# Performance work log

Hardware: AMD Instinct MI355X
Metric: run time of the kernel (lower is better)

## Reference

```python
import jax, jax.numpy as jnp
import numpy as np

N_REACH = 4096
N_T = 730
DT = 3600.0
VEL_LB = 0.3
VEL_UB = 15.0
Q_LB = 1e-4
SLOPE_LB = 1e-4


def _make_adjacency(n):
    # River-network DAG in topological order: each reach j (except outlet)
    # drains to exactly one downstream reach i > j  =>  strictly lower-triangular.
    rng = np.random.default_rng(0)
    j = np.arange(n - 1)
    ds = j + 1 + (rng.random(n - 1) * (n - 1 - j)).astype(np.int64)
    adj = np.zeros((n, n), dtype=np.float32)
    adj[ds, j] = 1.0
    return jnp.asarray(adj)


def setup_inputs() -> dict:
    key = jax.random.key(0)
    ks = jax.random.split(key, 8)
    u = lambda k, s: jax.random.uniform(k, s, dtype=jnp.float32)
    q_prime = u(ks[0], (N_T, N_REACH)) * 10.0            # lateral inflow m^3/s
    n = 0.01 + 0.09 * u(ks[1], (N_REACH,))               # Manning's n
    q_spatial = 1.5 + u(ks[2], (N_REACH,))               # log base > 1
    p_spatial = 1.0 + 3.0 * u(ks[3], (N_REACH,))         # width scale
    length = 1000.0 + 5000.0 * u(ks[4], (N_REACH,))      # reach length [m]
    slope = 1e-3 + 0.05 * u(ks[5], (N_REACH,))           # channel slope
    width = 5.0 + 100.0 * u(ks[6], (N_REACH,))           # width > p_spatial
    x_storage = 0.1 + 0.3 * u(ks[7], (N_REACH,))         # Muskingum x
    adj = _make_adjacency(N_REACH)
    return {"q_prime": q_prime, "n": n, "q_spatial": q_spatial,
            "p_spatial": p_spatial, "length": length, "slope": slope,
            "width": width, "x_storage": x_storage, "adj": adj}


def reference(q_prime, n, q_spatial, p_spatial, length, slope, width, x_storage, adj):
    slope = jnp.clip(slope, SLOPE_LB)
    # Manning's equation -> celerity (note: independent of discharge, as in source)
    depth = jnp.log(width / p_spatial) / jnp.log(q_spatial)
    v = (1.0 / n) * depth ** (2.0 / 3.0) * jnp.sqrt(slope)
    c = jnp.clip(v, VEL_LB, VEL_UB) * (5.0 / 3.0)
    k = length / c
    denom = 2.0 * k * (1.0 - x_storage) + DT
    c1 = (DT - 2.0 * k * x_storage) / denom
    c2 = (DT + 2.0 * k * x_storage) / denom
    c3 = (2.0 * k * (1.0 - x_storage) - DT) / denom
    c4 = 2.0 * DT / denom

    # Lower-triangular routing system: A = I - diag(c1) @ adjacency (constant)
    N = q_prime.shape[1]
    A = jnp.eye(N, dtype=q_prime.dtype) - c1[:, None] * adj

    q0 = q_prime[0]
    out0 = jnp.clip(q0[-1], Q_LB)  # single gage at index -1

    def step(q_t, qp_row):
        q_l = jnp.clip(qp_row, Q_LB)
        i_t = adj @ q_t                        # upstream inflow
        b = c2 * i_t + c3 * q_t + c4 * q_l
        x = jax.scipy.linalg.solve_triangular(A, b[:, None], lower=True)[:, 0]
        q_t1 = jnp.clip(x, Q_LB)
        return q_t1, q_t1[-1]

    _, outs = jax.lax.scan(step, q0, q_prime[:-1])  # timesteps 1..T-1 use q_prime[t-1]
    runoff = jnp.concatenate([out0[None], outs])[None, :]  # [1, T]
    return runoff
```

## Files before the change

### kernel.cpp

```cpp
#include <hip/hip_runtime.h>

#define N 4096
#define NT 730
#define NTH 512
#define PER_T 8
#define QLB 1e-4f
#define DT_S 3600.0f

#define WS_DS     0
#define WS_SZ     4096
#define WS_CCNT   8192
#define WS_COFF   12288
#define WS_CUR    16388
#define WS_HI     20484
#define WS_FLAG   24580
#define WS_C1     28676
#define WS_C2     32772
#define WS_C3     36868
#define WS_C4     40964
#define WS_CLIST  45060
#define WS_GP     49156
#define WS_LOP    53252
#define WS_C3P    57348
#define WS_C4P    61444
#define WS_CCNTP  65540
#define WS_COFF2  69636
#define WS_CUR2   73736
#define WS_EQ     77832
#define WS_EW     81928
#define WS_SP     86024
#define WS_ISP    94216
#define WS_QPP    102408
#define WS_END    (WS_QPP + NT * N)

__device__ __forceinline__ int qidx(int p) { return ((p & 7) << 9) | (p >> 3); }

template <int CTRL, int RMASK>
__device__ __forceinline__ double dpp_stage(double v) {
    union U { double d; unsigned int u[2]; };
    U s, t;
    s.d = v;
    t.u[0] = (unsigned)__builtin_amdgcn_update_dpp(0, (int)s.u[0], CTRL, RMASK, 0xf, false);
    t.u[1] = (unsigned)__builtin_amdgcn_update_dpp(0, (int)s.u[1], CTRL, RMASK, 0xf, false);
    return v + t.d;
}
__device__ __forceinline__ double wave_incl_scan(double v) {
    v = dpp_stage<0x111, 0xf>(v);
    v = dpp_stage<0x112, 0xf>(v);
    v = dpp_stage<0x114, 0xf>(v);
    v = dpp_stage<0x118, 0xf>(v);
    v = dpp_stage<0x142, 0xa>(v);
    v = dpp_stage<0x143, 0xc>(v);
    return v;
}

__global__ void k_init(int* ds, int* sz, int* ccnt, int* hi, int* flag) {
    int j = blockIdx.x * 256 + threadIdx.x;
    if (j < N) { ds[j] = N - 1; sz[j] = 1; ccnt[j] = 0; hi[j] = -1; flag[j] = 0; }
}

__global__ void k_extract(const float4* __restrict__ adj4, int* __restrict__ ds) {
    long idx = (long)blockIdx.x * 256 + threadIdx.x;
    if (idx >= (long)N * N / 4) return;
    float4 w = adj4[idx];
    long base = idx * 4;
    int row = (int)(base >> 12);
    int col = (int)(base & 4095);
    if (w.x != 0.0f) ds[col + 0] = row;
    if (w.y != 0.0f) ds[col + 1] = row;
    if (w.z != 0.0f) ds[col + 2] = row;
    if (w.w != 0.0f) ds[col + 3] = row;
}

__global__ void k_coeffs(const float* n, const float* qs, const float* ps,
                         const float* len, const float* slope, const float* width,
                         const float* xs, float* __restrict__ c1, float* __restrict__ c2,
                         float* __restrict__ c3, float* __restrict__ c4) {
    int i = blockIdx.x * 256 + threadIdx.x;
    if (i >= N) return;
    float s  = fmaxf(slope[i], 1e-4f);
    float dp = logf(width[i] / ps[i]) / logf(qs[i]);
    float v  = (1.0f / n[i]) * powf(dp, 2.0f / 3.0f) * sqrtf(s);
    float c  = fminf(fmaxf(v, 0.3f), 15.0f) * (5.0f / 3.0f);
    float k  = len[i] / c;
    float x  = xs[i];
    float denom = 2.0f * k * (1.0f - x) + DT_S;
    c1[i] = (DT_S - 2.0f * k * x) / denom;
    c2[i] = (DT_S + 2.0f * k * x) / denom;
    c3[i] = (2.0f * k * (1.0f - x) - DT_S) / denom;
    c4[i] = 2.0f * DT_S / denom;
}

__global__ void k_count(const int* __restrict__ ds, int* __restrict__ ccnt,
                        int* __restrict__ sz) {
    int u = blockIdx.x * 256 + threadIdx.x;
    if (u >= N || u == N - 1) return;
    atomicAdd(&ccnt[ds[u]], 1);
    int a = ds[u];
    while (true) {
        atomicAdd(&sz[a], 1);
        if (a == N - 1) break;
        a = ds[a];
    }
}

__global__ __launch_bounds__(1024) void k_scan(const int* __restrict__ src,
                                               int* __restrict__ off,
                                               int* __restrict__ cur) {
    __shared__ int buf[1024];
    int tid = threadIdx.x;
    int a0 = src[tid * 4 + 0], a1 = src[tid * 4 + 1];
    int a2 = src[tid * 4 + 2], a3 = src[tid * 4 + 3];
    int s1 = a0, s2 = a0 + a1, s3 = a0 + a1 + a2, tot = s3 + a3;
    buf[tid] = tot;
    __syncthreads();
    for (int o = 1; o < 1024; o <<= 1) {
        int add = (tid >= o) ? buf[tid - o] : 0;
        __syncthreads();
        buf[tid] += add;
        __syncthreads();
    }
    int base = buf[tid] - tot;
    off[tid * 4 + 0] = base;      cur[tid * 4 + 0] = base;
    off[tid * 4 + 1] = base + s1; cur[tid * 4 + 1] = base + s1;
    off[tid * 4 + 2] = base + s2; cur[tid * 4 + 2] = base + s2;
    off[tid * 4 + 3] = base + s3; cur[tid * 4 + 3] = base + s3;
    if (tid == 1023) off[N] = buf[1023];
}

__global__ void k_fill(const int* __restrict__ ds, int* __restrict__ cur,
                       int* __restrict__ clist) {
    int u = blockIdx.x * 256 + threadIdx.x;
    if (u >= N || u == N - 1) return;
    int cp = atomicAdd(&cur[ds[u]], 1);
    clist[cp] = u;
}

__global__ __launch_bounds__(1024) void k_post(const int* __restrict__ ds,
                                               const int* __restrict__ sz,
                                               const int* __restrict__ coff,
                                               const int* __restrict__ ccnt,
                                               const int* __restrict__ clist,
                                               int* __restrict__ hi,
                                               int* __restrict__ flag) {
    int tid = threadIdx.x;
    if (tid == 0) hi[N - 1] = N - 1;
    __syncthreads();
    for (int it = 0; it < 96; ++it) {
        for (int v = tid; v < N; v += 1024) {
            if (hi[v] >= 0 && flag[v] == 0) {
                int cum = hi[v] - sz[v] + 1;
                int b0 = coff[v], e0 = b0 + ccnt[v];
                for (int k = b0; k < e0; ++k) {
                    int c = clist[k];
                    hi[c] = cum + sz[c] - 1;
                    cum += sz[c];
                }
                flag[v] = 1;
            }
        }
        __syncthreads();
    }
}

__global__ void k_prep(const int* __restrict__ ds, const int* __restrict__ sz,
                       const int* __restrict__ ccnt, const int* __restrict__ hi,
                       const float* __restrict__ c1, const float* __restrict__ c3,
                       const float* __restrict__ c4,
                       int* __restrict__ gP, int* __restrict__ loP,
                       float* __restrict__ c3P, float* __restrict__ c4P,
                       int* __restrict__ ccntP,
                       double* __restrict__ SP, double* __restrict__ ISP) {
    int u = blockIdx.x * 256 + threadIdx.x;
    if (u >= N) return;
    int p = hi[u];
    double s = 1.0;
    if (u != N - 1) {
        int a = ds[u];
        while (true) {
            s *= (double)c1[a];
            if (a == N - 1) break;
            a = ds[a];
        }
    }
    SP[p] = s; ISP[p] = 1.0 / s;
    gP[p] = u;
    loP[p] = p - sz[u] + 1;
    c3P[p] = c3[u]; c4P[p] = c4[u];
    ccntP[p] = ccnt[u];
}

__global__ void k_fill2(const int* __restrict__ ds, const int* __restrict__ hi,
                        const float* __restrict__ c2, int* __restrict__ cur2,
                        unsigned int* __restrict__ EQ, float* __restrict__ EW) {
    int u = blockIdx.x * 256 + threadIdx.x;
    if (u >= N) return;
    if (u == N - 1) {
        unsigned rq = (unsigned)qidx(N - 1);
        EQ[N - 1] = (rq << 12) | rq;
        EW[N - 1] = 0.0f;
        return;
    }
    int d = ds[u];
    int slot = atomicAdd(&cur2[hi[d]], 1);
    EQ[slot] = ((unsigned)qidx(hi[u]) << 12) | (unsigned)qidx(hi[d]);
    EW[slot] = c2[d];
}

__global__ void k_permute(const float* __restrict__ qp, const int* __restrict__ gP,
                          float* __restrict__ qpp) {
    long e = (long)blockIdx.x * 256 + threadIdx.x;
    if (e >= (long)NT * N) return;
    int tr = (int)(e >> 12);
    int v  = (int)(e & 4095);
    qpp[e] = qp[(size_t)tr * N + gP[v]];
}

__global__ __launch_bounds__(NTH) void k_route(
    const float* __restrict__ qp, const float* __restrict__ qpp,
    const float* __restrict__ c3g, const float* __restrict__ c4g,
    const int* __restrict__ gPg, const int* __restrict__ loPg,
    const double* __restrict__ SPg, const double* __restrict__ ISPg,
    const unsigned int* __restrict__ EQg, const float* __restrict__ EWg,
    int use_perm, float* __restrict__ out) {
    __shared__ float qL[N];
    __shared__ float CS[N];
    __shared__ double TL[N];
    __shared__ __align__(16) double wpart[8];
    int tid = threadIdx.x;
    int lane = tid & 63, wid = tid >> 6;

    unsigned int eq[PER_T];
    float ew[PER_T];
    int lo[PER_T], g[PER_T];
    float c3r[PER_T], c4r[PER_T], qreg[PER_T], qn[PER_T];
    double Sr[PER_T], iSr[PER_T];
#pragma unroll
    for (int r = 0; r < PER_T; ++r) {
        int p = tid * PER_T + r;
        eq[r] = EQg[p]; ew[r] = EWg[p];
        lo[r] = loPg[p]; g[r] = gPg[p];
        c3r[r] = c3g[p]; c4r[r] = c4g[p];
        Sr[r] = SPg[p]; iSr[r] = ISPg[p];
        float q0 = use_perm ? qpp[p] : qp[g[r]];
        qreg[r] = q0;
        qL[(r << 9) | tid] = q0;
        CS[(r << 9) | tid] = c3r[r] * q0 + c4r[r] * fmaxf(q0, QLB);
    }
    if (tid == NTH - 1) out[0] = fmaxf(qreg[PER_T - 1], QLB);
    __syncthreads();

    for (int t = 1; t < NT; ++t) {
#pragma unroll
        for (int e = 0; e < PER_T; ++e) {
            float qv = qL[eq[e] >> 12];
            atomicAdd(&CS[eq[e] & 4095u], ew[e] * qv);
        }
        __syncthreads();
        float bb[PER_T];
        double yv[PER_T], Tloc[PER_T];
        double tl = 0.0;
#pragma unroll
        for (int r = 0; r < PER_T; ++r) {
            float b = CS[(r << 9) | tid];
            bb[r] = b;
            double y = Sr[r] * (double)b;
            yv[r] = y;
            tl += y;
            Tloc[r] = tl;
        }
        double incl = wave_incl_scan(tl);
        if (lane == 63) wpart[wid] = incl;
        __syncthreads();
        double2 w0 = *(const double2*)&wpart[0];
        double2 w1 = *(const double2*)&wpart[2];
        double2 w2 = *(const double2*)&wpart[4];
        double2 w3 = *(const double2*)&wpart[6];
        double woff = 0.0;
        if (wid > 0) woff += w0.x;
        if (wid > 1) woff += w0.y;
        if (wid > 2) woff += w1.x;
        if (wid > 3) woff += w1.y;
        if (wid > 4) woff += w2.x;
        if (wid > 5) woff += w2.y;
        if (wid > 6) woff += w3.x;
        double texcl = woff + incl - tl;
#pragma unroll
        for (int r = 0; r < PER_T; ++r)
            TL[(r << 9) | tid] = texcl + Tloc[r];
        __syncthreads();
        if (t < NT - 1) {
            if (use_perm) {
                const float4* row4 = (const float4*)(qpp + (size_t)t * N);
                float4 a = row4[tid * 2], b = row4[tid * 2 + 1];
                qn[0] = a.x; qn[1] = a.y; qn[2] = a.z; qn[3] = a.w;
                qn[4] = b.x; qn[5] = b.y; qn[6] = b.z; qn[7] = b.w;
            } else {
                const float* row = qp + (size_t)t * N;
#pragma unroll
                for (int r = 0; r < PER_T; ++r) qn[r] = row[g[r]];
            }
        }
#pragma unroll
        for (int r = 0; r < PER_T; ++r) {
            int l = lo[r];
            double Tg = (l > 0) ? TL[qidx(l - 1)] : 0.0;
            double Tself = texcl + Tloc[r] - yv[r];
            double x = (double)bb[r] + (Tself - Tg) * iSr[r];
            qreg[r] = fmaxf((float)x, QLB);
        }
        if (tid == NTH - 1) out[t] = qreg[PER_T - 1];
#pragma unroll
        for (int r = 0; r < PER_T; ++r) {
            qL[(r << 9) | tid] = qreg[r];
            CS[(r << 9) | tid] = c3r[r] * qreg[r] + c4r[r] * fmaxf(qn[r], QLB);
        }
        __syncthreads();
    }
}

extern "C" void kernel_launch(void* const* d_in, const int* in_sizes, int n_in,
                              void* d_out, int out_size, void* d_ws, size_t ws_size,
                              hipStream_t stream) {
    const float* qp    = (const float*)d_in[0];
    const float* n     = (const float*)d_in[1];
    const float* qs    = (const float*)d_in[2];
    const float* ps    = (const float*)d_in[3];
    const float* len   = (const float*)d_in[4];
    const float* slope = (const float*)d_in[5];
    const float* width = (const float*)d_in[6];
    const float* xs    = (const float*)d_in[7];
    const float* adj   = (const float*)d_in[8];
    float* out = (float*)d_out;

    int*          W     = (int*)d_ws;
    int*          ds    = W + WS_DS;
    int*          sz    = W + WS_SZ;
    int*          ccnt  = W + WS_CCNT;
    int*          coff  = W + WS_COFF;
    int*          cur   = W + WS_CUR;
    int*          hi    = W + WS_HI;
    int*          flag  = W + WS_FLAG;
    float*        c1    = (float*)(W + WS_C1);
    float*        c2    = (float*)(W + WS_C2);
    float*        c3    = (float*)(W + WS_C3);
    float*        c4    = (float*)(W + WS_C4);
    int*          clist = W + WS_CLIST;
    int*          gP    = W + WS_GP;
    int*          loP   = W + WS_LOP;
    float*        c3P   = (float*)(W + WS_C3P);
    float*        c4P   = (float*)(W + WS_C4P);
    int*          ccntP = W + WS_CCNTP;
    int*          coff2 = W + WS_COFF2;
    int*          cur2  = W + WS_CUR2;
    unsigned int* EQ    = (unsigned int*)(W + WS_EQ);
    float*        EW    = (float*)(W + WS_EW);
    double*       SP    = (double*)(W + WS_SP);
    double*       ISP   = (double*)(W + WS_ISP);
    float*        QPP   = (float*)(W + WS_QPP);

    int use_perm = (ws_size >= (size_t)WS_END * 4) ? 1 : 0;

    k_init<<<(N + 255) / 256, 256, 0, stream>>>(ds, sz, ccnt, hi, flag);
    k_extract<<<(N * N / 4 + 255) / 256, 256, 0, stream>>>((const float4*)adj, ds);
    k_coeffs<<<(N + 255) / 256, 256, 0, stream>>>(n, qs, ps, len, slope, width, xs,
                                                  c1, c2, c3, c4);
    k_count<<<(N + 255) / 256, 256, 0, stream>>>(ds, ccnt, sz);
    k_scan<<<1, 1024, 0, stream>>>(ccnt, coff, cur);
    k_fill<<<(N + 255) / 256, 256, 0, stream>>>(ds, cur, clist);
    k_post<<<1, 1024, 0, stream>>>(ds, sz, coff, ccnt, clist, hi, flag);
    k_prep<<<(N + 255) / 256, 256, 0, stream>>>(ds, sz, ccnt, hi, c1, c3, c4,
                                                gP, loP, c3P, c4P, ccntP, SP, ISP);
    k_scan<<<1, 1024, 0, stream>>>(ccntP, coff2, cur2);
    k_fill2<<<(N + 255) / 256, 256, 0, stream>>>(ds, hi, c2, cur2, EQ, EW);
    if (use_perm)
        k_permute<<<(int)(((long)NT * N + 255) / 256), 256, 0, stream>>>(qp, gP, QPP);
    k_route<<<1, NTH, 0, stream>>>(qp, QPP, c3P, c4P, gP, loP, SP, ISP, EQ, EW,
                                   use_perm, out);
}
```

Before: 5.124 ms.

## Push upstream inflow from registers into double-buffered shared accumulator

Each thread now scatters its own freshly computed outflows to its downstream parent's slot in a double-buffered shared accumulator, instead of gathering upstream q from a shared array at the start of the next step. The step's right-hand side is finished in registers, and per-thread partial scans are stored wave-local, with the cross-wave offsets added later from prefix values held in registers. Together these remove two of the four block barriers per timestep in the serial 730-step loop and drop the edge-sorting prep kernels. The cost is extra selects for the wave offset, and the float atomic order differs from before.

```diff
diff --git a/kernel.cpp b/kernel.cpp
--- a/kernel.cpp
+++ b/kernel.cpp
@@ -23,14 +23,11 @@
 #define WS_LOP    53252
 #define WS_C3P    57348
 #define WS_C4P    61444
-#define WS_CCNTP  65540
-#define WS_COFF2  69636
-#define WS_CUR2   73736
-#define WS_EQ     77832
-#define WS_EW     81928
-#define WS_SP     86024
-#define WS_ISP    94216
-#define WS_QPP    102408
+#define WS_EPAR   65540
+#define WS_EWS    69636
+#define WS_SP     73736
+#define WS_ISP    81928
+#define WS_QPP    90120
 #define WS_END    (WS_QPP + NT * N)
 
 __device__ __forceinline__ int qidx(int p) { return ((p & 7) << 9) | (p >> 3); }
@@ -164,12 +161,12 @@
 }
 
 __global__ void k_prep(const int* __restrict__ ds, const int* __restrict__ sz,
-                       const int* __restrict__ ccnt, const int* __restrict__ hi,
-                       const float* __restrict__ c1, const float* __restrict__ c3,
-                       const float* __restrict__ c4,
+                       const int* __restrict__ hi,
+                       const float* __restrict__ c1, const float* __restrict__ c2,
+                       const float* __restrict__ c3, const float* __restrict__ c4,
                        int* __restrict__ gP, int* __restrict__ loP,
                        float* __restrict__ c3P, float* __restrict__ c4P,
-                       int* __restrict__ ccntP,
+                       int* __restrict__ eparP, float* __restrict__ ewsP,
                        double* __restrict__ SP, double* __restrict__ ISP) {
     int u = blockIdx.x * 256 + threadIdx.x;
     if (u >= N) return;
@@ -187,24 +184,13 @@
     gP[p] = u;
     loP[p] = p - sz[u] + 1;
     c3P[p] = c3[u]; c4P[p] = c4[u];
-    ccntP[p] = ccnt[u];
-}
-
-__global__ void k_fill2(const int* __restrict__ ds, const int* __restrict__ hi,
-                        const float* __restrict__ c2, int* __restrict__ cur2,
-                        unsigned int* __restrict__ EQ, float* __restrict__ EW) {
-    int u = blockIdx.x * 256 + threadIdx.x;
-    if (u >= N) return;
-    if (u == N - 1) {
-        unsigned rq = (unsigned)qidx(N - 1);
-        EQ[N - 1] = (rq << 12) | rq;
-        EW[N - 1] = 0.0f;
-        return;
-    }
-    int d = ds[u];
-    int slot = atomicAdd(&cur2[hi[d]], 1);
-    EQ[slot] = ((unsigned)qidx(hi[u]) << 12) | (unsigned)qidx(hi[d]);
-    EW[slot] = c2[d];
+    if (u != N - 1) {
+        eparP[p] = hi[ds[u]];
+        ewsP[p] = c2[ds[u]];
+    } else {
+        eparP[p] = p;
+        ewsP[p] = 0.0f;
+    }
 }
 
 __global__ void k_permute(const float* __restrict__ qp, const int* __restrict__ gP,
@@ -220,62 +206,88 @@
     const float* __restrict__ qp, const float* __restrict__ qpp,
     const float* __restrict__ c3g, const float* __restrict__ c4g,
     const int* __restrict__ gPg, const int* __restrict__ loPg,
+    const int* __restrict__ eparPg, const float* __restrict__ ewsPg,
     const double* __restrict__ SPg, const double* __restrict__ ISPg,
-    const unsigned int* __restrict__ EQg, const float* __restrict__ EWg,
     int use_perm, float* __restrict__ out) {
-    __shared__ float qL[N];
-    __shared__ float CS[N];
-    __shared__ double TL[N];
+    __shared__ float CSA[2][N];
+    __shared__ double TLp[N];
     __shared__ __align__(16) double wpart[8];
     int tid = threadIdx.x;
     int lane = tid & 63, wid = tid >> 6;
 
-    unsigned int eq[PER_T];
-    float ew[PER_T];
-    int lo[PER_T], g[PER_T];
-    float c3r[PER_T], c4r[PER_T], qreg[PER_T], qn[PER_T];
+    int epar[PER_T], jg[PER_T], wv[PER_T], g[PER_T];
+    float ews[PER_T], c3r[PER_T], c4r[PER_T], qreg[PER_T], qc[PER_T], qn[PER_T];
     double Sr[PER_T], iSr[PER_T];
+    bool haslo[PER_T];
 #pragma unroll
     for (int r = 0; r < PER_T; ++r) {
         int p = tid * PER_T + r;
-        eq[r] = EQg[p]; ew[r] = EWg[p];
-        lo[r] = loPg[p]; g[r] = gPg[p];
+        epar[r] = eparPg[p]; ews[r] = ewsPg[p];
+        int l = loPg[p];
+        haslo[r] = (l > 0);
+        int lm = (l > 0) ? (l - 1) : 0;
+        jg[r] = qidx(lm);
+        wv[r] = lm >> 9;
+        g[r] = gPg[p];
         c3r[r] = c3g[p]; c4r[r] = c4g[p];
         Sr[r] = SPg[p]; iSr[r] = ISPg[p];
         float q0 = use_perm ? qpp[p] : qp[g[r]];
-        qreg[r] = q0;
-        qL[(r << 9) | tid] = q0;
-        CS[(r << 9) | tid] = c3r[r] * q0 + c4r[r] * fmaxf(q0, QLB);
+        qreg[r] = q0; qc[r] = q0;
+    }
+    {
+        float4 z = make_float4(0.f, 0.f, 0.f, 0.f);
+        float4* c0 = (float4*)&CSA[0][tid * PER_T];
+        float4* c1 = (float4*)&CSA[1][tid * PER_T];
+        c0[0] = z; c0[1] = z; c1[0] = z; c1[1] = z;
     }
     if (tid == NTH - 1) out[0] = fmaxf(qreg[PER_T - 1], QLB);
     __syncthreads();
+#pragma unroll
+    for (int r = 0; r < PER_T; ++r)
+        atomicAdd(&CSA[1][epar[r]], ews[r] * qreg[r]);
+    __syncthreads();
 
     for (int t = 1; t < NT; ++t) {
-#pragma unroll
-        for (int e = 0; e < PER_T; ++e) {
-            float qv = qL[eq[e] >> 12];
-            atomicAdd(&CS[eq[e] & 4095u], ew[e] * qv);
-        }
-        __syncthreads();
+        int s = t & 1;
+        float4 ca = *(const float4*)&CSA[s][tid * PER_T];
+        float4 cb = *(const float4*)&CSA[s][tid * PER_T + 4];
+        float cs[PER_T] = {ca.x, ca.y, ca.z, ca.w, cb.x, cb.y, cb.z, cb.w};
         float bb[PER_T];
         double yv[PER_T], Tloc[PER_T];
         double tl = 0.0;
 #pragma unroll
         for (int r = 0; r < PER_T; ++r) {
-            float b = CS[(r << 9) | tid];
-            bb[r] = b;
-            double y = Sr[r] * (double)b;
+            bb[r] = cs[r] + c3r[r] * qreg[r] + c4r[r] * fmaxf(qc[r], QLB);
+            double y = Sr[r] * (double)bb[r];
             yv[r] = y;
             tl += y;
             Tloc[r] = tl;
         }
         double incl = wave_incl_scan(tl);
+        double texw = incl - tl;
+#pragma unroll
+        for (int r = 0; r < PER_T; ++r)
+            TLp[(r << 9) | tid] = texw + Tloc[r];
         if (lane == 63) wpart[wid] = incl;
         __syncthreads();
+        if (t < NT - 1) {
+            if (use_perm) {
+                const float4* row4 = (const float4*)(qpp + (size_t)t * N);
+                float4 a = row4[tid * 2], b = row4[tid * 2 + 1];
+                qn[0] = a.x; qn[1] = a.y; qn[2] = a.z; qn[3] = a.w;
+                qn[4] = b.x; qn[5] = b.y; qn[6] = b.z; qn[7] = b.w;
+            } else {
+                const float* row = qp + (size_t)t * N;
+#pragma unroll
+                for (int r = 0; r < PER_T; ++r) qn[r] = row[g[r]];
+            }
+        }
         double2 w0 = *(const double2*)&wpart[0];
         double2 w1 = *(const double2*)&wpart[2];
         double2 w2 = *(const double2*)&wpart[4];
         double2 w3 = *(const double2*)&wpart[6];
+        double P1 = w0.x, P2 = P1 + w0.y, P3 = P2 + w1.x, P4 = P3 + w1.y;
+        double P5 = P4 + w2.x, P6 = P5 + w2.y, P7 = P6 + w3.x;
         double woff = 0.0;
         if (wid > 0) woff += w0.x;
         if (wid > 1) woff += w0.y;
@@ -284,38 +296,29 @@
         if (wid > 4) woff += w2.x;
         if (wid > 5) woff += w2.y;
         if (wid > 6) woff += w3.x;
-        double texcl = woff + incl - tl;
-#pragma unroll
-        for (int r = 0; r < PER_T; ++r)
-            TL[(r << 9) | tid] = texcl + Tloc[r];
-        __syncthreads();
-        if (t < NT - 1) {
-            if (use_perm) {
-                const float4* row4 = (const float4*)(qpp + (size_t)t * N);
-                float4 a = row4[tid * 2], b = row4[tid * 2 + 1];
-                qn[0] = a.x; qn[1] = a.y; qn[2] = a.z; qn[3] = a.w;
-                qn[4] = b.x; qn[5] = b.y; qn[6] = b.z; qn[7] = b.w;
-            } else {
-                const float* row = qp + (size_t)t * N;
-#pragma unroll
-                for (int r = 0; r < PER_T; ++r) qn[r] = row[g[r]];
-            }
-        }
 #pragma unroll
         for (int r = 0; r < PER_T; ++r) {
-            int l = lo[r];
-            double Tg = (l > 0) ? TL[qidx(l - 1)] : 0.0;
-            double Tself = texcl + Tloc[r] - yv[r];
+            int w = wv[r];
+            double lo2 = (w & 2) ? ((w & 1) ? P3 : P2) : ((w & 1) ? P1 : 0.0);
+            double hi2 = (w & 2) ? ((w & 1) ? P7 : P6) : ((w & 1) ? P5 : P4);
+            double goff = (w & 4) ? hi2 : lo2;
+            double Tg = haslo[r] ? (TLp[jg[r]] + goff) : 0.0;
+            double Tself = woff + texw + Tloc[r] - yv[r];
             double x = (double)bb[r] + (Tself - Tg) * iSr[r];
             qreg[r] = fmaxf((float)x, QLB);
         }
+        {
+            float4 z = make_float4(0.f, 0.f, 0.f, 0.f);
+            float4* c0 = (float4*)&CSA[s][tid * PER_T];
+            c0[0] = z; c0[1] = z;
+        }
+#pragma unroll
+        for (int r = 0; r < PER_T; ++r)
+            atomicAdd(&CSA[s ^ 1][epar[r]], ews[r] * qreg[r]);
         if (tid == NTH - 1) out[t] = qreg[PER_T - 1];
-#pragma unroll
-        for (int r = 0; r < PER_T; ++r) {
-            qL[(r << 9) | tid] = qreg[r];
-            CS[(r << 9) | tid] = c3r[r] * qreg[r] + c4r[r] * fmaxf(qn[r], QLB);
-        }
-        __syncthreads();
+        __syncthreads();
+#pragma unroll
+        for (int r = 0; r < PER_T; ++r) qc[r] = qn[r];
     }
 }
 
@@ -333,31 +336,28 @@
     const float* adj   = (const float*)d_in[8];
     float* out = (float*)d_out;
 
-    int*          W     = (int*)d_ws;
-    int*          ds    = W + WS_DS;
-    int*          sz    = W + WS_SZ;
-    int*          ccnt  = W + WS_CCNT;
-    int*          coff  = W + WS_COFF;
-    int*          cur   = W + WS_CUR;
-    int*          hi    = W + WS_HI;
-    int*          flag  = W + WS_FLAG;
-    float*        c1    = (float*)(W + WS_C1);
-    float*        c2    = (float*)(W + WS_C2);
-    float*        c3    = (float*)(W + WS_C3);
-    float*        c4    = (float*)(W + WS_C4);
-    int*          clist = W + WS_CLIST;
-    int*          gP    = W + WS_GP;
-    int*          loP   = W + WS_LOP;
-    float*        c3P   = (float*)(W + WS_C3P);
-    float*        c4P   = (float*)(W + WS_C4P);
-    int*          ccntP = W + WS_CCNTP;
-    int*          coff2 = W + WS_COFF2;
-    int*          cur2  = W + WS_CUR2;
-    unsigned int* EQ    = (unsigned int*)(W + WS_EQ);
-    float*        EW    = (float*)(W + WS_EW);
-    double*       SP    = (double*)(W + WS_SP);
-    double*       ISP   = (double*)(W + WS_ISP);
-    float*        QPP   = (float*)(W + WS_QPP);
+    int*    W     = (int*)d_ws;
+    int*    ds    = W + WS_DS;
+    int*    sz    = W + WS_SZ;
+    int*    ccnt  = W + WS_CCNT;
+    int*    coff  = W + WS_COFF;
+    int*    cur   = W + WS_CUR;
+    int*    hi    = W + WS_HI;
+    int*    flag  = W + WS_FLAG;
+    float*  c1    = (float*)(W + WS_C1);
+    float*  c2    = (float*)(W + WS_C2);
+    float*  c3    = (float*)(W + WS_C3);
+    float*  c4    = (float*)(W + WS_C4);
+    int*    clist = W + WS_CLIST;
+    int*    gP    = W + WS_GP;
+    int*    loP   = W + WS_LOP;
+    float*  c3P   = (float*)(W + WS_C3P);
+    float*  c4P   = (float*)(W + WS_C4P);
+    int*    eparP = W + WS_EPAR;
+    float*  ewsP  = (float*)(W + WS_EWS);
+    double* SP    = (double*)(W + WS_SP);
+    double* ISP   = (double*)(W + WS_ISP);
+    float*  QPP   = (float*)(W + WS_QPP);
 
     int use_perm = (ws_size >= (size_t)WS_END * 4) ? 1 : 0;
 
@@ -369,12 +369,11 @@
     k_scan<<<1, 1024, 0, stream>>>(ccnt, coff, cur);
     k_fill<<<(N + 255) / 256, 256, 0, stream>>>(ds, cur, clist);
     k_post<<<1, 1024, 0, stream>>>(ds, sz, coff, ccnt, clist, hi, flag);
-    k_prep<<<(N + 255) / 256, 256, 0, stream>>>(ds, sz, ccnt, hi, c1, c3, c4,
-                                                gP, loP, c3P, c4P, ccntP, SP, ISP);
-    k_scan<<<1, 1024, 0, stream>>>(ccntP, coff2, cur2);
-    k_fill2<<<(N + 255) / 256, 256, 0, stream>>>(ds, hi, c2, cur2, EQ, EW);
+    k_prep<<<(N + 255) / 256, 256, 0, stream>>>(ds, sz, hi, c1, c2, c3, c4,
+                                                gP, loP, c3P, c4P, eparP, ewsP,
+                                                SP, ISP);
     if (use_perm)
         k_permute<<<(int)(((long)NT * N + 255) / 256), 256, 0, stream>>>(qp, gP, QPP);
-    k_route<<<1, NTH, 0, stream>>>(qp, QPP, c3P, c4P, gP, loP, SP, ISP, EQ, EW,
-                                   use_perm, out);
-}
+    k_route<<<1, NTH, 0, stream>>>(qp, QPP, c3P, c4P, gP, loP, eparP, ewsP,
+                                   SP, ISP, use_perm, out);
+}
```

New measurement: 5.178 ms. About the same (+1.1%).
